# Performance work log

Measured on AMD Instinct MI355X. Metric: run time of the kernel, lower is better.

The kernel has to match this reference:

```python
import jax, jax.numpy as jnp
import numpy as np

B, N_L, C, NH = 8, 256, 256, 8
HH, WW = 64, 64
N_C = HH * WW
L = 3  # focal_level
KS = [3, 5, 7]  # focal kernel sizes: focal_factor*k + focal_window
HD = C // NH
SCALE = HD ** -0.5


def _dwconv(x, w, k):
    # x: [B,C,H,W], w: [C,1,k,k] depthwise (groups=C)
    p = k // 2
    return jax.lax.conv_general_dilated(
        x, w, window_strides=(1, 1), padding=[(p, p), (p, p)],
        feature_group_count=C,
        dimension_numbers=('NCHW', 'OIHW', 'NCHW'))


def setup_inputs() -> dict:
    key = jax.random.key(0)
    ks = jax.random.split(key, 16)
    s = 0.02
    inp = {
        'latents': jax.random.normal(ks[0], (B, N_L, C), jnp.float32),
        'context': jax.random.normal(ks[1], (B, N_C, C), jnp.float32),
        'q_w': jax.random.normal(ks[2], (C, C), jnp.float32) * s,
        'k_w': jax.random.normal(ks[3], (C, C), jnp.float32) * s,
        'f_w': jax.random.normal(ks[4], (C + L + 1, C), jnp.float32) * s,
        'f_b': jnp.zeros((C + L + 1,), jnp.float32),
        'h_w': jax.random.normal(ks[5], (C, C), jnp.float32) * s,
        'h_b': jnp.zeros((C,), jnp.float32),
        'fk0': jax.random.normal(ks[6], (C, 1, KS[0], KS[0]), jnp.float32) * s,
        'fk1': jax.random.normal(ks[7], (C, 1, KS[1], KS[1]), jnp.float32) * s,
        'fk2': jax.random.normal(ks[8], (C, 1, KS[2], KS[2]), jnp.float32) * s,
        'proj_w': jax.random.normal(ks[9], (C, C), jnp.float32) * s,
        'proj_b': jnp.zeros((C,), jnp.float32),
        'H': HH,
        'W': WW,
    }
    return inp


def reference(latents, context, q_w, k_w, f_w, f_b, h_w, h_b,
              fk0, fk1, fk2, proj_w, proj_b, H, W):
    gelu = lambda x: jax.nn.gelu(x, approximate=False)
    # attention scores
    q = (latents @ q_w.T).reshape(B, N_L, NH, HD).transpose(0, 2, 1, 3)  # [B,NH,Nl,HD]
    k = (context @ k_w.T).reshape(B, N_C, NH, HD).transpose(0, 2, 1, 3)  # [B,NH,Nc,HD]
    attn = jax.nn.softmax(jnp.einsum('bhnd,bhmd->bhnm', q, k) * SCALE, axis=-1)
    # focal modulation on context
    f_out = context.reshape(B, H, W, C) @ f_w.T + f_b          # [B,H,W,C+L+1]
    f_out = f_out.transpose(0, 3, 1, 2)                        # [B,C+L+1,H,W]
    v_ctx, gates = f_out[:, :C], f_out[:, C:]
    v_ctx_all = jnp.zeros_like(v_ctx)
    for l, fk in enumerate((fk0, fk1, fk2)):
        v_ctx = gelu(_dwconv(v_ctx, fk, KS[l]))
        v_ctx_all = v_ctx_all + v_ctx * gates[:, l:l + 1]
    v_global = gelu(v_ctx.mean(axis=(2, 3), keepdims=True))
    v_ctx_all = v_ctx_all + v_global * gates[:, L:L + 1]
    # 1x1 conv modulator
    v_mod = jnp.einsum('bchw,dc->bdhw', v_ctx_all, h_w) + h_b[None, :, None, None]
    # NOTE: faithful to original -- raw reshape of NCHW tensor (no permute)
    v = v_mod.reshape(B, N_C, NH, HD).transpose(0, 2, 1, 3)    # [B,NH,Nc,HD]
    out = jnp.einsum('bhnm,bhmd->bhnd', attn, v)               # [B,NH,Nl,HD]
    out = out.transpose(0, 2, 1, 3).reshape(B, N_L, C)
    out = out @ proj_w.T + proj_b
    return out, attn
```

## Files before the change

kernel.cpp:

```cpp
#include <hip/hip_runtime.h>
#include <math.h>


namespace {

constexpr float CSCALE = 0.17677669529663688f;

typedef __attribute__((ext_vector_type(8))) __bf16 bf16x8;
typedef __attribute__((ext_vector_type(4))) float f32x4;

__device__ __forceinline__ float gelu_f(float x) {
  return 0.5f * x * (1.0f + erff(x * 0.70710678118654752f));
}

__device__ __forceinline__ unsigned short f2bf(float f) {
  union { float f; unsigned u; } v; v.f = f;
  unsigned r = v.u + 0x7fffu + ((v.u >> 16) & 1u);
  return (unsigned short)(r >> 16);
}

__device__ __forceinline__ float bf2f(unsigned short u) {
  union { unsigned u; float f; } v; v.u = (unsigned)u << 16;
  return v.f;
}

__global__ __launch_bounds__(256) void cast_all(
    const float* __restrict__ ctx, const float* __restrict__ lat,
    const float* __restrict__ qw, const float* __restrict__ kw,
    const float* __restrict__ fw, const float* __restrict__ hww,
    const float* __restrict__ pw,
    unsigned short* ctxb, unsigned short* latb, unsigned short* qwb,
    unsigned short* kwb, unsigned short* fwb, unsigned short* hwb,
    unsigned short* pwb) {
  const int blk = blockIdx.x;
  const float* s; unsigned short* d; int b0, nq;
  if      (blk < 2048) { s = ctx; d = ctxb; b0 = blk;        nq = 2097152; }
  else if (blk < 2176) { s = lat; d = latb; b0 = blk - 2048; nq = 131072; }
  else if (blk < 2192) { s = qw;  d = qwb;  b0 = blk - 2176; nq = 16384; }
  else if (blk < 2208) { s = kw;  d = kwb;  b0 = blk - 2192; nq = 16384; }
  else if (blk < 2225) { s = fw;  d = fwb;  b0 = blk - 2208; nq = 16640; }
  else if (blk < 2241) { s = hww; d = hwb;  b0 = blk - 2225; nq = 16384; }
  else                 { s = pw;  d = pwb;  b0 = blk - 2241; nq = 16384; }
  #pragma unroll
  for (int t = 0; t < 4; ++t) {
    const int q = b0*1024 + t*256 + threadIdx.x;
    if (q < nq) {
      float4 v = ((const float4*)s)[q];
      ushort4 o;
      o.x = f2bf(v.x); o.y = f2bf(v.y); o.z = f2bf(v.z); o.w = f2bf(v.w);
      ((ushort4*)d)[q] = o;
    }
  }
}

__global__ __launch_bounds__(256) void mfma_qk(
    const unsigned short* __restrict__ A, const unsigned short* __restrict__ W,
    unsigned short* __restrict__ out) {
  const int r0 = blockIdx.x * 64, n0 = blockIdx.y * 64;
  const int tid = threadIdx.x, w = tid >> 6, l = tid & 63;
  const int lr = l & 15, lk = l >> 4;
  const int rw = r0 + w*16;
  const unsigned short* ap = A + (size_t)(rw + lr)*256 + lk*8;
  f32x4 acc[4] = {{0.f,0.f,0.f,0.f},{0.f,0.f,0.f,0.f},{0.f,0.f,0.f,0.f},{0.f,0.f,0.f,0.f}};
  #pragma unroll
  for (int k0 = 0; k0 < 256; k0 += 32) {
    bf16x8 a = *reinterpret_cast<const bf16x8*>(ap + k0);
    #pragma unroll
    for (int j = 0; j < 4; ++j) {
      bf16x8 b = *reinterpret_cast<const bf16x8*>(W + (size_t)(n0 + j*16 + lr)*256 + k0 + lk*8);
      acc[j] = __builtin_amdgcn_mfma_f32_16x16x32_bf16(a, b, acc[j], 0, 0, 0);
    }
  }
  #pragma unroll
  for (int j = 0; j < 4; ++j)
    #pragma unroll
    for (int rr = 0; rr < 4; ++rr)
      out[(size_t)(rw + lk*4 + rr)*256 + n0 + j*16 + lr] = f2bf(acc[j][rr]);
}

__global__ __launch_bounds__(256) void mfma_f(
    const unsigned short* __restrict__ A, const unsigned short* __restrict__ W,
    const float* __restrict__ fb, unsigned short* __restrict__ vctx,
    float* __restrict__ gates) {
  const int r0 = blockIdx.x * 64, n0 = blockIdx.y * 64;
  const int tid = threadIdx.x, w = tid >> 6, l = tid & 63;
  const int lr = l & 15, lk = l >> 4;
  const int rw = r0 + w*16;
  const unsigned short* ap = A + (size_t)(rw + lr)*256 + lk*8;
  f32x4 acc[4] = {{0.f,0.f,0.f,0.f},{0.f,0.f,0.f,0.f},{0.f,0.f,0.f,0.f},{0.f,0.f,0.f,0.f}};
  #pragma unroll
  for (int k0 = 0; k0 < 256; k0 += 32) {
    bf16x8 a = *reinterpret_cast<const bf16x8*>(ap + k0);
    #pragma unroll
    for (int j = 0; j < 4; ++j) {
      const int n = n0 + j*16 + lr;
      bf16x8 b = {};
      if (n < 260)
        b = *reinterpret_cast<const bf16x8*>(W + (size_t)n*256 + k0 + lk*8);
      acc[j] = __builtin_amdgcn_mfma_f32_16x16x32_bf16(a, b, acc[j], 0, 0, 0);
    }
  }
  const int rbase = rw + lk*4;
  const int b = rbase >> 12, hw = rbase & 4095;
  #pragma unroll
  for (int j = 0; j < 4; ++j) {
    const int n = n0 + j*16 + lr;
    if (n >= 260) continue;
    const float bb = fb[n];
    if (n < 256) {
      ushort4 o;
      o.x = f2bf(acc[j][0] + bb); o.y = f2bf(acc[j][1] + bb);
      o.z = f2bf(acc[j][2] + bb); o.w = f2bf(acc[j][3] + bb);
      *(ushort4*)&vctx[((size_t)(b*256 + n))*4096 + hw] = o;
    } else {
      float4 o = make_float4(acc[j][0] + bb, acc[j][1] + bb,
                             acc[j][2] + bb, acc[j][3] + bb);
      *(float4*)&gates[((size_t)(b*4 + (n - 256)))*4096 + hw] = o;
    }
  }
}

__global__ __launch_bounds__(256) void fused_conv(
    const unsigned short* in, const float* __restrict__ wk3,
    const float* __restrict__ wk5, const float* __restrict__ wk7,
    const float* __restrict__ gates, unsigned short* out) {
  constexpr int TW = 70;
  __shared__ float A[TW * TW];
  __shared__ float w3[9];
  __shared__ float w5[25];
  __shared__ float w7[49];
  __shared__ float red[4];
  const int tid = threadIdx.x;
  const int b = blockIdx.x >> 8, c = blockIdx.x & 255;
  if (tid < 9)  w3[tid] = wk3[c*9  + tid];
  else if (tid < 34) w5[tid-9]  = wk5[c*25 + tid-9];
  else if (tid < 83) w7[tid-34] = wk7[c*49 + tid-34];
  const unsigned short* ip = in + (size_t)(b*256 + c) * 4096;
  for (int idx = tid; idx < TW*TW; idx += 256) {
    const int ty = idx / TW, tx = idx - ty*TW;
    const int gy = ty - 3, gx = tx - 3;
    A[idx] = (gy >= 0 && gy < 64 && gx >= 0 && gx < 64) ? bf2f(ip[gy*64 + gx]) : 0.0f;
  }
  __syncthreads();
  const float* g0 = gates + (size_t)(b*4 + 0) * 4096;
  const float* g1 = gates + (size_t)(b*4 + 1) * 4096;
  const float* g2 = gates + (size_t)(b*4 + 2) * 4096;
  const float* g3 = gates + (size_t)(b*4 + 3) * 4096;
  float v[16], acc[16];
  #pragma unroll
  for (int ii = 0; ii < 16; ++ii) {
    const int pix = ii*256 + tid;
    const int y = pix >> 6, x = pix & 63;
    float s = 0.f;
    #pragma unroll
    for (int ky = 0; ky < 3; ++ky)
      #pragma unroll
      for (int kx = 0; kx < 3; ++kx)
        s += w3[ky*3 + kx] * A[(y+2+ky)*TW + (x+2+kx)];
    v[ii] = gelu_f(s);
    acc[ii] = v[ii] * g0[pix];
  }
  __syncthreads();
  #pragma unroll
  for (int ii = 0; ii < 16; ++ii) {
    const int pix = ii*256 + tid;
    A[((pix >> 6) + 3)*TW + (pix & 63) + 3] = v[ii];
  }
  __syncthreads();
  #pragma unroll
  for (int ii = 0; ii < 16; ++ii) {
    const int pix = ii*256 + tid;
    const int y = pix >> 6, x = pix & 63;
    float s = 0.f;
    #pragma unroll
    for (int ky = 0; ky < 5; ++ky)
      #pragma unroll
      for (int kx = 0; kx < 5; ++kx)
        s += w5[ky*5 + kx] * A[(y+1+ky)*TW + (x+1+kx)];
    v[ii] = gelu_f(s);
    acc[ii] += v[ii] * g1[pix];
  }
  __syncthreads();
  #pragma unroll
  for (int ii = 0; ii < 16; ++ii) {
    const int pix = ii*256 + tid;
    A[((pix >> 6) + 3)*TW + (pix & 63) + 3] = v[ii];
  }
  __syncthreads();
  float msum = 0.f;
  #pragma unroll
  for (int ii = 0; ii < 16; ++ii) {
    const int pix = ii*256 + tid;
    const int y = pix >> 6, x = pix & 63;
    float s = 0.f;
    #pragma unroll
    for (int ky = 0; ky < 7; ++ky)
      #pragma unroll
      for (int kx = 0; kx < 7; ++kx)
        s += w7[ky*7 + kx] * A[(y+ky)*TW + (x+kx)];
    v[ii] = gelu_f(s);
    acc[ii] += v[ii] * g2[pix];
    msum += v[ii];
  }
  #pragma unroll
  for (int off = 32; off >= 1; off >>= 1) msum += __shfl_xor(msum, off, 64);
  if ((tid & 63) == 0) red[tid >> 6] = msum;
  __syncthreads();
  const float vg = gelu_f((red[0]+red[1]+red[2]+red[3]) * (1.0f/4096.0f));
  unsigned short* vp = out + (size_t)(b*256 + c) * 4096;
  #pragma unroll
  for (int ii = 0; ii < 16; ++ii) {
    const int pix = ii*256 + tid;
    vp[pix] = f2bf(acc[ii] + vg * g3[pix]);
  }
}

__global__ __launch_bounds__(256) void mfma_h(
    const unsigned short* __restrict__ vall, const unsigned short* __restrict__ hwb,
    const float* __restrict__ hb, unsigned short* __restrict__ vt) {
  __shared__ unsigned short Bs[64][264];
  const int hw0 = blockIdx.x * 64, d0 = blockIdx.y * 64, b = blockIdx.z;
  const int tid = threadIdx.x, w = tid >> 6, l = tid & 63;
  const int lr = l & 15, lk = l >> 4;
  const int cl = tid >> 3, hl = (tid & 7) * 8;
  #pragma unroll
  for (int c0 = 0; c0 < 256; c0 += 32) {
    const unsigned short* sp = vall + (size_t)(b*256 + c0 + cl)*4096 + hw0 + hl;
    ushort4 u0 = *(const ushort4*)sp;
    ushort4 u1 = *(const ushort4*)(sp + 4);
    Bs[hl+0][c0+cl] = u0.x; Bs[hl+1][c0+cl] = u0.y;
    Bs[hl+2][c0+cl] = u0.z; Bs[hl+3][c0+cl] = u0.w;
    Bs[hl+4][c0+cl] = u1.x; Bs[hl+5][c0+cl] = u1.y;
    Bs[hl+6][c0+cl] = u1.z; Bs[hl+7][c0+cl] = u1.w;
  }
  __syncthreads();
  const int dw = d0 + w*16;
  const unsigned short* ap = hwb + (size_t)(dw + lr)*256 + lk*8;
  f32x4 acc[4] = {{0.f,0.f,0.f,0.f},{0.f,0.f,0.f,0.f},{0.f,0.f,0.f,0.f},{0.f,0.f,0.f,0.f}};
  #pragma unroll
  for (int k0 = 0; k0 < 256; k0 += 32) {
    bf16x8 a = *reinterpret_cast<const bf16x8*>(ap + k0);
    #pragma unroll
    for (int j = 0; j < 4; ++j) {
      bf16x8 bv = *reinterpret_cast<const bf16x8*>(&Bs[j*16 + lr][k0 + lk*8]);
      acc[j] = __builtin_amdgcn_mfma_f32_16x16x32_bf16(a, bv, acc[j], 0, 0, 0);
    }
  }
  const int q = hw0 >> 8, dim0 = hw0 & 255;
  float hbv[4];
  #pragma unroll
  for (int rr = 0; rr < 4; ++rr) hbv[rr] = hb[dw + lk*4 + rr];
  #pragma unroll
  for (int j = 0; j < 4; ++j) {
    const int dim = dim0 + j*16 + lr;
    unsigned short* vrow = vt + ((size_t)(b*256 + dim))*4096 + q;
    #pragma unroll
    for (int rr = 0; rr < 4; ++rr) {
      const int d = dw + lk*4 + rr;
      vrow[d*16] = f2bf(acc[j][rr] + hbv[rr]);
    }
  }
}

__global__ __launch_bounds__(256) void attn_pv(
    const unsigned short* __restrict__ qb, const unsigned short* __restrict__ kb,
    const unsigned short* __restrict__ vt, float* __restrict__ attn,
    unsigned short* __restrict__ aout) {
  const int blk = blockIdx.x;
  const int bh = blk & 63, nt = blk >> 6;
  const int b = bh >> 3, h = bh & 7;
  const int tid = threadIdx.x;
  const int w = tid >> 6, l = tid & 63;
  const int lr = l & 15, lk = l >> 4;
  const int n0 = nt * 16;
  __shared__ float rs[4][16];
  __shared__ unsigned short pl[4][16][40];
  __shared__ float osum[4][16][32];
  bf16x8 aq = *reinterpret_cast<const bf16x8*>(
      qb + ((size_t)(b*256 + n0 + lr))*256 + h*32 + lk*8);
  const unsigned short* kbase = kb + (size_t)b*4096*256 + h*32 + lk*8;
  float sum[4] = {0.f, 0.f, 0.f, 0.f};
  #pragma unroll 2
  for (int mt = 0; mt < 64; ++mt) {
    const int m0 = w*1024 + mt*16;
    bf16x8 bk = *reinterpret_cast<const bf16x8*>(kbase + (size_t)(m0 + lr)*256);
    f32x4 d = __builtin_amdgcn_mfma_f32_16x16x32_bf16(aq, bk, (f32x4){0.f,0.f,0.f,0.f}, 0, 0, 0);
    #pragma unroll
    for (int r = 0; r < 4; ++r) sum[r] += __expf(d[r] * CSCALE);
  }
  #pragma unroll
  for (int r = 0; r < 4; ++r) {
    #pragma unroll
    for (int m = 1; m < 16; m <<= 1) sum[r] += __shfl_xor(sum[r], m, 64);
  }
  if (lr == 0) {
    #pragma unroll
    for (int r = 0; r < 4; ++r) rs[w][lk*4 + r] = sum[r];
  }
  __syncthreads();
  float invS[4];
  #pragma unroll
  for (int r = 0; r < 4; ++r) {
    const int rowi = lk*4 + r;
    invS[r] = 1.0f / (rs[0][rowi] + rs[1][rowi] + rs[2][rowi] + rs[3][rowi]);
  }
  float* ab = attn + ((size_t)bh*256 + n0) * 4096;
  const unsigned short* vb = vt + ((size_t)(b*256 + h*32))*4096;
  f32x4 acc0 = {0.f,0.f,0.f,0.f}, acc1 = {0.f,0.f,0.f,0.f};
  for (int mt = 0; mt < 64; ++mt) {
    const int m0 = w*1024 + mt*16;
    bf16x8 bk = *reinterpret_cast<const bf16x8*>(kbase + (size_t)(m0 + lr)*256);
    f32x4 d = __builtin_amdgcn_mfma_f32_16x16x32_bf16(aq, bk, (f32x4){0.f,0.f,0.f,0.f}, 0, 0, 0);
    const int mo = (mt & 1) << 4;
    #pragma unroll
    for (int r = 0; r < 4; ++r) {
      const float p = __expf(d[r] * CSCALE) * invS[r];
      ab[(size_t)(lk*4 + r)*4096 + m0 + lr] = p;
      pl[w][lk*4 + r][mo + lr] = f2bf(p);
    }
    if (mt & 1) {
      const int mb = w*1024 + (mt - 1)*16;
      bf16x8 pa = *reinterpret_cast<const bf16x8*>(&pl[w][lr][lk*8]);
      bf16x8 bv0 = *reinterpret_cast<const bf16x8*>(vb + (size_t)lr*4096 + mb + lk*8);
      bf16x8 bv1 = *reinterpret_cast<const bf16x8*>(vb + (size_t)(16 + lr)*4096 + mb + lk*8);
      acc0 = __builtin_amdgcn_mfma_f32_16x16x32_bf16(pa, bv0, acc0, 0, 0, 0);
      acc1 = __builtin_amdgcn_mfma_f32_16x16x32_bf16(pa, bv1, acc1, 0, 0, 0);
    }
  }
  #pragma unroll
  for (int r = 0; r < 4; ++r) {
    osum[w][lk*4 + r][lr]      = acc0[r];
    osum[w][lk*4 + r][16 + lr] = acc1[r];
  }
  __syncthreads();
  for (int i = tid; i < 512; i += 256) {
    const int n = i >> 5, d = i & 31;
    const float s = osum[0][n][d] + osum[1][n][d] + osum[2][n][d] + osum[3][n][d];
    aout[((size_t)(b*256 + n0 + n))*256 + h*32 + d] = f2bf(s);
  }
}

__global__ __launch_bounds__(256) void mfma_proj(
    const unsigned short* __restrict__ A, const unsigned short* __restrict__ W,
    const float* __restrict__ pb, float* __restrict__ out) {
  const int r0 = blockIdx.x * 64, n0 = blockIdx.y * 64;
  const int tid = threadIdx.x, w = tid >> 6, l = tid & 63;
  const int lr = l & 15, lk = l >> 4;
  const int rw = r0 + w*16;
  const unsigned short* ap = A + (size_t)(rw + lr)*256 + lk*8;
  f32x4 acc[4] = {{0.f,0.f,0.f,0.f},{0.f,0.f,0.f,0.f},{0.f,0.f,0.f,0.f},{0.f,0.f,0.f,0.f}};
  #pragma unroll
  for (int k0 = 0; k0 < 256; k0 += 32) {
    bf16x8 a = *reinterpret_cast<const bf16x8*>(ap + k0);
    #pragma unroll
    for (int j = 0; j < 4; ++j) {
      bf16x8 b = *reinterpret_cast<const bf16x8*>(W + (size_t)(n0 + j*16 + lr)*256 + k0 + lk*8);
      acc[j] = __builtin_amdgcn_mfma_f32_16x16x32_bf16(a, b, acc[j], 0, 0, 0);
    }
  }
  #pragma unroll
  for (int j = 0; j < 4; ++j) {
    const int n = n0 + j*16 + lr;
    const float bb = pb[n];
    #pragma unroll
    for (int rr = 0; rr < 4; ++rr)
      out[(size_t)(rw + lk*4 + rr)*256 + n] = acc[j][rr] + bb;
  }
}

}

extern "C" void kernel_launch(void* const* d_in, const int* in_sizes, int n_in,
                              void* d_out, int out_size, void* d_ws, size_t ws_size,
                              hipStream_t stream) {
  (void)in_sizes; (void)n_in; (void)out_size; (void)ws_size;
  const float* latents = (const float*)d_in[0];
  const float* context = (const float*)d_in[1];
  const float* q_w    = (const float*)d_in[2];
  const float* k_w    = (const float*)d_in[3];
  const float* f_w    = (const float*)d_in[4];
  const float* f_b    = (const float*)d_in[5];
  const float* h_w    = (const float*)d_in[6];
  const float* h_b    = (const float*)d_in[7];
  const float* fk0    = (const float*)d_in[8];
  const float* fk1    = (const float*)d_in[9];
  const float* fk2    = (const float*)d_in[10];
  const float* proj_w = (const float*)d_in[11];
  const float* proj_b = (const float*)d_in[12];

  float* out0 = (float*)d_out;
  float* attn = out0 + (size_t)8*256*256;

  char* w = (char*)d_ws;
  unsigned short* ctx_bf = (unsigned short*)(w + 0x0);
  unsigned short* vcv    = (unsigned short*)(w + 0x1000000);
  unsigned short* k_bf   = (unsigned short*)(w + 0x2100000);
  unsigned short* v_tb   = (unsigned short*)(w + 0x3100000);
  unsigned short* q_bf   = (unsigned short*)(w + 0x4100000);
  unsigned short* lat_bf = (unsigned short*)(w + 0x4200000);
  unsigned short* qw_bf  = (unsigned short*)(w + 0x4300000);
  unsigned short* kw_bf  = (unsigned short*)(w + 0x4340000);
  unsigned short* fw_bf  = (unsigned short*)(w + 0x4380000);
  unsigned short* hw_bf  = (unsigned short*)(w + 0x43C0000);
  unsigned short* pw_bf  = (unsigned short*)(w + 0x4400000);
  float*          gates  = (float*)(w + 0x4440000);
  unsigned short* aout_bf= (unsigned short*)(w + 0x44C0000);

  cast_all<<<2257, 256, 0, stream>>>(context, latents, q_w, k_w, f_w, h_w, proj_w,
                                     ctx_bf, lat_bf, qw_bf, kw_bf, fw_bf, hw_bf, pw_bf);
  mfma_qk  <<<dim3(32, 4),  256, 0, stream>>>(lat_bf, qw_bf, q_bf);
  mfma_qk  <<<dim3(512, 4), 256, 0, stream>>>(ctx_bf, kw_bf, k_bf);
  mfma_f   <<<dim3(512, 5), 256, 0, stream>>>(ctx_bf, fw_bf, f_b, vcv, gates);
  fused_conv<<<2048, 256, 0, stream>>>(vcv, fk0, fk1, fk2, gates, vcv);
  mfma_h   <<<dim3(64, 4, 8), 256, 0, stream>>>(vcv, hw_bf, h_b, v_tb);
  attn_pv  <<<1024, 256, 0, stream>>>(q_bf, k_bf, v_tb, attn, aout_bf);
  mfma_proj<<<dim3(32, 4), 256, 0, stream>>>(aout_bf, pw_bf, proj_b, out0);
}
```

Measured before the change: 386.4 us.

## Coalesce attn and V writes via LDS staging, merge K and focal GEMMs

Merges the K projection and focal projection GEMMs into one launch over a 9-wide grid, so the context tile is shared in cache and one launch is saved. The mfma_h epilogue now stages results in LDS and writes rows linearly, then a new transpose kernel produces the transposed V layout with 16-byte stores, replacing scattered 2-byte strided stores. attn_pv stages the fp32 probabilities in LDS and writes the attn matrix as 32-wide contiguous rows instead of 16-element fragments. The cost is an extra kernel, an extra intermediate buffer round trip, more LDS use and extra syncs.

After: 342.4 us. 1.13x faster.

```diff
diff --git a/kernel.cpp b/kernel.cpp
--- a/kernel.cpp
+++ b/kernel.cpp
@@ -78,11 +78,15 @@
       out[(size_t)(rw + lk*4 + rr)*256 + n0 + j*16 + lr] = f2bf(acc[j][rr]);
 }
 
-__global__ __launch_bounds__(256) void mfma_f(
-    const unsigned short* __restrict__ A, const unsigned short* __restrict__ W,
-    const float* __restrict__ fb, unsigned short* __restrict__ vctx,
+__global__ __launch_bounds__(256) void mfma_fk(
+    const unsigned short* __restrict__ A, const unsigned short* __restrict__ Wk,
+    const unsigned short* __restrict__ Wf, const float* __restrict__ fb,
+    unsigned short* __restrict__ kout, unsigned short* __restrict__ vctx,
     float* __restrict__ gates) {
-  const int r0 = blockIdx.x * 64, n0 = blockIdx.y * 64;
+  const int r0 = blockIdx.x * 64;
+  const bool isk = blockIdx.y < 4;
+  const int n0 = (isk ? blockIdx.y : blockIdx.y - 4) * 64;
+  const unsigned short* W = isk ? Wk : Wf;
   const int tid = threadIdx.x, w = tid >> 6, l = tid & 63;
   const int lr = l & 15, lk = l >> 4;
   const int rw = r0 + w*16;
@@ -95,27 +99,35 @@
     for (int j = 0; j < 4; ++j) {
       const int n = n0 + j*16 + lr;
       bf16x8 b = {};
-      if (n < 260)
+      if (isk || n < 260)
         b = *reinterpret_cast<const bf16x8*>(W + (size_t)n*256 + k0 + lk*8);
       acc[j] = __builtin_amdgcn_mfma_f32_16x16x32_bf16(a, b, acc[j], 0, 0, 0);
     }
   }
-  const int rbase = rw + lk*4;
-  const int b = rbase >> 12, hw = rbase & 4095;
-  #pragma unroll
-  for (int j = 0; j < 4; ++j) {
-    const int n = n0 + j*16 + lr;
-    if (n >= 260) continue;
-    const float bb = fb[n];
-    if (n < 256) {
-      ushort4 o;
-      o.x = f2bf(acc[j][0] + bb); o.y = f2bf(acc[j][1] + bb);
-      o.z = f2bf(acc[j][2] + bb); o.w = f2bf(acc[j][3] + bb);
-      *(ushort4*)&vctx[((size_t)(b*256 + n))*4096 + hw] = o;
-    } else {
-      float4 o = make_float4(acc[j][0] + bb, acc[j][1] + bb,
-                             acc[j][2] + bb, acc[j][3] + bb);
-      *(float4*)&gates[((size_t)(b*4 + (n - 256)))*4096 + hw] = o;
+  if (isk) {
+    #pragma unroll
+    for (int j = 0; j < 4; ++j)
+      #pragma unroll
+      for (int rr = 0; rr < 4; ++rr)
+        kout[(size_t)(rw + lk*4 + rr)*256 + n0 + j*16 + lr] = f2bf(acc[j][rr]);
+  } else {
+    const int rbase = rw + lk*4;
+    const int b = rbase >> 12, hw = rbase & 4095;
+    #pragma unroll
+    for (int j = 0; j < 4; ++j) {
+      const int n = n0 + j*16 + lr;
+      if (n >= 260) continue;
+      const float bb = fb[n];
+      if (n < 256) {
+        ushort4 o;
+        o.x = f2bf(acc[j][0] + bb); o.y = f2bf(acc[j][1] + bb);
+        o.z = f2bf(acc[j][2] + bb); o.w = f2bf(acc[j][3] + bb);
+        *(ushort4*)&vctx[((size_t)(b*256 + n))*4096 + hw] = o;
+      } else {
+        float4 o = make_float4(acc[j][0] + bb, acc[j][1] + bb,
+                               acc[j][2] + bb, acc[j][3] + bb);
+        *(float4*)&gates[((size_t)(b*4 + (n - 256)))*4096 + hw] = o;
+      }
     }
   }
 }
@@ -217,8 +229,9 @@
 
 __global__ __launch_bounds__(256) void mfma_h(
     const unsigned short* __restrict__ vall, const unsigned short* __restrict__ hwb,
-    const float* __restrict__ hb, unsigned short* __restrict__ vt) {
+    const float* __restrict__ hb, unsigned short* __restrict__ vlin) {
   __shared__ unsigned short Bs[64][264];
+  __shared__ unsigned short Ts[64][72];
   const int hw0 = blockIdx.x * 64, d0 = blockIdx.y * 64, b = blockIdx.z;
   const int tid = threadIdx.x, w = tid >> 6, l = tid & 63;
   const int lr = l & 15, lk = l >> 4;
@@ -246,19 +259,47 @@
       acc[j] = __builtin_amdgcn_mfma_f32_16x16x32_bf16(a, bv, acc[j], 0, 0, 0);
     }
   }
+  float hbv[4];
+  #pragma unroll
+  for (int rr = 0; rr < 4; ++rr) hbv[rr] = hb[dw + lk*4 + rr];
+  #pragma unroll
+  for (int j = 0; j < 4; ++j)
+    #pragma unroll
+    for (int rr = 0; rr < 4; ++rr)
+      Ts[w*16 + lk*4 + rr][j*16 + lr] = f2bf(acc[j][rr] + hbv[rr]);
+  __syncthreads();
   const int q = hw0 >> 8, dim0 = hw0 & 255;
-  float hbv[4];
-  #pragma unroll
-  for (int rr = 0; rr < 4; ++rr) hbv[rr] = hb[dw + lk*4 + rr];
-  #pragma unroll
-  for (int j = 0; j < 4; ++j) {
-    const int dim = dim0 + j*16 + lr;
-    unsigned short* vrow = vt + ((size_t)(b*256 + dim))*4096 + q;
-    #pragma unroll
-    for (int rr = 0; rr < 4; ++rr) {
-      const int d = dw + lk*4 + rr;
-      vrow[d*16] = f2bf(acc[j][rr] + hbv[rr]);
-    }
+  #pragma unroll
+  for (int it = 0; it < 2; ++it) {
+    const int dl = it*32 + (tid >> 3);
+    const int ch = tid & 7;
+    const int m = (d0 + dl)*16 + q;
+    uint4 v = *(const uint4*)&Ts[dl][ch*8];
+    *(uint4*)&vlin[((size_t)(b*4096 + m))*256 + dim0 + ch*8] = v;
+  }
+}
+
+__global__ __launch_bounds__(256) void trans_bf(
+    const unsigned short* __restrict__ vlin, unsigned short* __restrict__ vt) {
+  __shared__ unsigned short T[64][72];
+  const int tid = threadIdx.x;
+  const int m0 = blockIdx.x * 64, d0 = blockIdx.y * 64, b = blockIdx.z;
+  #pragma unroll
+  for (int it = 0; it < 2; ++it) {
+    const int ml = it*32 + (tid >> 3);
+    const int ch = tid & 7;
+    uint4 v = *(const uint4*)&vlin[((size_t)(b*4096 + m0 + ml))*256 + d0 + ch*8];
+    *(uint4*)&T[ml][ch*8] = v;
+  }
+  __syncthreads();
+  #pragma unroll
+  for (int it = 0; it < 2; ++it) {
+    const int dl = it*32 + (tid >> 3);
+    const int ch = tid & 7;
+    unsigned short tmp[8];
+    #pragma unroll
+    for (int k = 0; k < 8; ++k) tmp[k] = T[ch*8 + k][dl];
+    *(uint4*)&vt[((size_t)(b*256 + d0 + dl))*4096 + m0 + ch*8] = *(uint4*)tmp;
   }
 }
 
@@ -275,6 +316,7 @@
   const int n0 = nt * 16;
   __shared__ float rs[4][16];
   __shared__ unsigned short pl[4][16][40];
+  __shared__ float ps[4][16][34];
   __shared__ float osum[4][16][32];
   bf16x8 aq = *reinterpret_cast<const bf16x8*>(
       qb + ((size_t)(b*256 + n0 + lr))*256 + h*32 + lk*8);
@@ -306,6 +348,8 @@
   }
   float* ab = attn + ((size_t)bh*256 + n0) * 4096;
   const unsigned short* vb = vt + ((size_t)(b*256 + h*32))*4096;
+  const int fr = l >> 5;
+  const int fm = l & 31;
   f32x4 acc0 = {0.f,0.f,0.f,0.f}, acc1 = {0.f,0.f,0.f,0.f};
   for (int mt = 0; mt < 64; ++mt) {
     const int m0 = w*1024 + mt*16;
@@ -315,7 +359,7 @@
     #pragma unroll
     for (int r = 0; r < 4; ++r) {
       const float p = __expf(d[r] * CSCALE) * invS[r];
-      ab[(size_t)(lk*4 + r)*4096 + m0 + lr] = p;
+      ps[w][lk*4 + r][mo + lr] = p;
       pl[w][lk*4 + r][mo + lr] = f2bf(p);
     }
     if (mt & 1) {
@@ -325,6 +369,11 @@
       bf16x8 bv1 = *reinterpret_cast<const bf16x8*>(vb + (size_t)(16 + lr)*4096 + mb + lk*8);
       acc0 = __builtin_amdgcn_mfma_f32_16x16x32_bf16(pa, bv0, acc0, 0, 0, 0);
       acc1 = __builtin_amdgcn_mfma_f32_16x16x32_bf16(pa, bv1, acc1, 0, 0, 0);
+      #pragma unroll
+      for (int i = 0; i < 8; ++i) {
+        const int row = i*2 + fr;
+        ab[(size_t)row*4096 + mb + fm] = ps[w][row][fm];
+      }
     }
   }
   #pragma unroll
@@ -405,14 +454,15 @@
   unsigned short* pw_bf  = (unsigned short*)(w + 0x4400000);
   float*          gates  = (float*)(w + 0x4440000);
   unsigned short* aout_bf= (unsigned short*)(w + 0x44C0000);
+  unsigned short* vlin_bf= (unsigned short*)(w + 0x4600000);
 
   cast_all<<<2257, 256, 0, stream>>>(context, latents, q_w, k_w, f_w, h_w, proj_w,
                                      ctx_bf, lat_bf, qw_bf, kw_bf, fw_bf, hw_bf, pw_bf);
   mfma_qk  <<<dim3(32, 4),  256, 0, stream>>>(lat_bf, qw_bf, q_bf);
-  mfma_qk  <<<dim3(512, 4), 256, 0, stream>>>(ctx_bf, kw_bf, k_bf);
-  mfma_f   <<<dim3(512, 5), 256, 0, stream>>>(ctx_bf, fw_bf, f_b, vcv, gates);
+  mfma_fk  <<<dim3(512, 9), 256, 0, stream>>>(ctx_bf, kw_bf, fw_bf, f_b, k_bf, vcv, gates);
   fused_conv<<<2048, 256, 0, stream>>>(vcv, fk0, fk1, fk2, gates, vcv);
-  mfma_h   <<<dim3(64, 4, 8), 256, 0, stream>>>(vcv, hw_bf, h_b, v_tb);
+  mfma_h   <<<dim3(64, 4, 8), 256, 0, stream>>>(vcv, hw_bf, h_b, vlin_bf);
+  trans_bf <<<dim3(64, 4, 8), 256, 0, stream>>>(vlin_bf, v_tb);
   attn_pv  <<<1024, 256, 0, stream>>>(q_bf, k_bf, v_tb, attn, aout_bf);
   mfma_proj<<<dim3(32, 4), 256, 0, stream>>>(aout_bf, pw_bf, proj_b, out0);
 }
```
